# Optimization experiments

Hardware: AMD Instinct MI355X
Metric: run time of the kernel (lower is better)

Reference implementation:

```python
import jax, jax.numpy as jnp
import numpy as np

KERNEL_SIZE = 15


def setup_inputs() -> dict:
    key = jax.random.key(0)
    k1, k2 = jax.random.split(key)
    N, H, W = 16, 512, 512
    x = jax.random.normal(k1, (N, N, H, W), dtype=jnp.float32)
    kernel = jax.random.uniform(k2, (N, N, KERNEL_SIZE, KERNEL_SIZE), dtype=jnp.float32)
    return {"x": x, "kernel": kernel}


def reference(x, kernel):
    # x: (N, C, H, W) with b == c == N; kernel: (N, N, k, k)
    k = kernel.shape[-1]
    p = k // 2
    xs = x[:, 0:1, :, :]  # only channel 0 is used: (N, 1, H, W)
    xp = jnp.pad(xs, ((0, 0), (0, 0), (p, p), (p, p)), mode="reflect")  # ReflectionPad2d

    def per_sample(im, ker):
        # im: (1, Hp, Wp), ker: (N, k, k) -> conv of one image with N kernels
        o = jax.lax.conv_general_dilated(
            im[None],              # (1, 1, Hp, Wp)
            ker[:, None],          # (N, 1, k, k)
            window_strides=(1, 1),
            padding="VALID",
            dimension_numbers=("NCHW", "OIHW", "NCHW"),
        )[0]                       # (N, H, W)
        return o / jnp.max(o)      # global max-normalize per sample

    res = jax.vmap(per_sample)(xp, kernel)   # (i=N, j=N, H, W); res[i, j] = conv(x_i, kernel[i, j]) / max_j
    # original writes out[j, i] = res[i, j]
    return jnp.transpose(res, (1, 0, 2, 3))
```

## Files before the change

### kernel.cpp

```cpp
#include <hip/hip_runtime.h>

typedef __bf16 bf16x8 __attribute__((ext_vector_type(8)));
typedef float f32x4 __attribute__((ext_vector_type(4)));
typedef unsigned int u32;
typedef unsigned short u16;

#define PDIM 528
#define PIMG (PDIM * PDIM)
#define IN_STRIDE 56
#define IN_ROWS   31

__device__ __forceinline__ u16 f2bf(float f) {
    u32 u = __builtin_bit_cast(u32, f);
    return (u16)((u + 0x7FFFu + ((u >> 16) & 1u)) >> 16);
}
__device__ __forceinline__ int refl(int i) {
    return i < 0 ? -i : (i > 511 ? 1022 - i : i);
}

__global__ __launch_bounds__(256) void cvtpad(const float* __restrict__ x,
                                              u16* __restrict__ P) {
    const int u  = blockIdx.x * 256 + threadIdx.x;
    const int n  = u / (PDIM * 66);
    const int r  = u - n * (PDIM * 66);
    const int pr = r / 66;
    const int cs = r - pr * 66;
    const int pc0 = cs * 8;
    const float* sx = x + (size_t)n * (16u * 512u * 512u) + (size_t)refl(pr - 7) * 512;
    const int g0 = pc0 - 8;
    float v[8];
    if (g0 >= 0 && g0 <= 504) {
        const float4 a = *(const float4*)(sx + g0);
        const float4 b = *(const float4*)(sx + g0 + 4);
        v[0] = a.x; v[1] = a.y; v[2] = a.z; v[3] = a.w;
        v[4] = b.x; v[5] = b.y; v[6] = b.z; v[7] = b.w;
    } else {
        #pragma unroll
        for (int i = 0; i < 8; ++i) v[i] = sx[refl(g0 + i)];
    }
    uint4 q;
    q.x = (u32)f2bf(v[0]) | ((u32)f2bf(v[1]) << 16);
    q.y = (u32)f2bf(v[2]) | ((u32)f2bf(v[3]) << 16);
    q.z = (u32)f2bf(v[4]) | ((u32)f2bf(v[5]) << 16);
    q.w = (u32)f2bf(v[6]) | ((u32)f2bf(v[7]) << 16);
    *(uint4*)(P + (size_t)n * PIMG + (size_t)pr * PDIM + pc0) = q;
}

__global__ __launch_bounds__(256) void packkern(const float* __restrict__ kern,
                                                uint4* __restrict__ afragG) {
    const int u = blockIdx.x * 256 + threadIdx.x;
    const int n    = u >> 9;
    const int rem  = u & 511;
    const int ks   = rem >> 6;
    const int lane = rem & 63;
    const int oca = lane & 15, g = lane >> 4, g1 = g & 1, g2 = g >> 1;
    const float* kp = kern + ((size_t)n * 16 + oca) * 225;
    const int kh = 2 * ks + g2;
    u16 b[8];
    #pragma unroll
    for (int j = 0; j < 8; ++j) {
        const int kw = 8 * g1 + j;
        b[j] = f2bf((kh < 15 && kw < 15) ? kp[kh * 15 + kw] : 0.f);
    }
    uint4 q;
    q.x = (u32)b[0] | ((u32)b[1] << 16);
    q.y = (u32)b[2] | ((u32)b[3] << 16);
    q.z = (u32)b[4] | ((u32)b[5] << 16);
    q.w = (u32)b[6] | ((u32)b[7] << 16);
    afragG[u] = q;
}

template <int MODE>
__global__ __launch_bounds__(256) void dynconv(const u16* __restrict__ P,
                                               const uint4* __restrict__ afragG,
                                               float* __restrict__ out,
                                               float* __restrict__ partial) {
    __shared__ __align__(16) u16 lds_in[IN_ROWS * IN_STRIDE];
    __shared__ float wm[4];

    const int tid  = threadIdx.x;
    const int lane = tid & 63;
    const int wave = tid >> 6;
    const int c0 = blockIdx.x * 32;
    const int h0 = blockIdx.y * 16;
    const int n  = blockIdx.z;

    if (tid < IN_ROWS * 6) {
        const int rr  = tid / 6;
        const int cs8 = tid - rr * 6;
        const uint4 q = *(const uint4*)(P + (size_t)n * PIMG
                                        + (size_t)(h0 + rr) * PDIM + c0 + 8 * cs8);
        *(uint4*)&lds_in[rr * IN_STRIDE + 8 * cs8] = q;
    }

    const int g  = lane >> 4;
    const int g1 = g & 1;
    const int g2 = g >> 1;
    bf16x8 afrag[8];
    {
        const uint4* ap = afragG + ((size_t)n << 9) + lane;
        #pragma unroll
        for (int ks = 0; ks < 8; ++ks)
            afrag[ks] = __builtin_bit_cast(bf16x8, ap[ks << 6]);
    }

    float scale = 0.f;
    if constexpr (MODE == 1) {
        const float* pp = partial + n * 512 + lane * 8;
        const float4 a = *(const float4*)pp;
        const float4 b = *(const float4*)(pp + 4);
        float pv = fmaxf(fmaxf(fmaxf(a.x, a.y), fmaxf(a.z, a.w)),
                         fmaxf(fmaxf(b.x, b.y), fmaxf(b.z, b.w)));
        #pragma unroll
        for (int off = 32; off > 0; off >>= 1) pv = fmaxf(pv, __shfl_xor(pv, off, 64));
        scale = 1.0f / pv;
    }

    __syncthreads();

    const int hh = lane & 15;
    const char* lbase = (const char*)lds_in
                        + (hh + g2) * (IN_STRIDE * 2) + 16 * (wave + g1);

    f32x4 acc[8];
    #pragma unroll
    for (int t = 0; t < 8; ++t) acc[t] = f32x4{0.f, 0.f, 0.f, 0.f};

    u32 Ea[8], Eb[8];
#define LDE(E, ks) do {                                                        \
        const uint4 _a = *(const uint4*)(lbase + (ks) * (2 * IN_STRIDE * 2));  \
        const uint4 _b = *(const uint4*)(lbase + (ks) * (2 * IN_STRIDE * 2) + 16); \
        E[0] = _a.x; E[1] = _a.y; E[2] = _a.z; E[3] = _a.w;                    \
        E[4] = _b.x; E[5] = _b.y; E[6] = _b.z; E[7] = _b.w; } while (0)
#define KSTEP(E, ks) do {                                                      \
        _Pragma("unroll")                                                      \
        for (int t = 0; t < 8; ++t) {                                          \
            const int s = t + 1, xb = s >> 1;                                  \
            u32 d0, d1, d2, d3;                                                \
            if (s & 1) {                                                       \
                d0 = __builtin_amdgcn_alignbit(E[xb + 1], E[xb], 16);          \
                d1 = __builtin_amdgcn_alignbit(E[xb + 2], E[xb + 1], 16);      \
                d2 = __builtin_amdgcn_alignbit(E[xb + 3], E[xb + 2], 16);      \
                d3 = __builtin_amdgcn_alignbit(E[xb + 4], E[xb + 3], 16);      \
            } else { d0 = E[xb]; d1 = E[xb + 1]; d2 = E[xb + 2]; d3 = E[xb + 3]; } \
            uint4 dv; dv.x = d0; dv.y = d1; dv.z = d2; dv.w = d3;              \
            acc[t] = __builtin_amdgcn_mfma_f32_16x16x32_bf16(                  \
                afrag[ks], __builtin_bit_cast(bf16x8, dv), acc[t], 0, 0, 0);   \
        } } while (0)

    LDE(Ea, 0);
    LDE(Eb, 1); KSTEP(Ea, 0);
    LDE(Ea, 2); KSTEP(Eb, 1);
    LDE(Eb, 3); KSTEP(Ea, 2);
    LDE(Ea, 4); KSTEP(Eb, 3);
    LDE(Eb, 5); KSTEP(Ea, 4);
    LDE(Ea, 6); KSTEP(Eb, 5);
    LDE(Eb, 7); KSTEP(Ea, 6);
    KSTEP(Eb, 7);
#undef LDE
#undef KSTEP

    if constexpr (MODE == 0) {
        float m = -3.4e38f;
        #pragma unroll
        for (int t = 0; t < 8; ++t)
            #pragma unroll
            for (int r = 0; r < 4; ++r) m = fmaxf(m, acc[t][r]);
        #pragma unroll
        for (int off = 32; off > 0; off >>= 1) m = fmaxf(m, __shfl_xor(m, off, 64));
        if (lane == 0) wm[wave] = m;
        __syncthreads();
        if (tid == 0)
            partial[n * 512 + blockIdx.y * 16 + blockIdx.x] =
                fmaxf(fmaxf(wm[0], wm[1]), fmaxf(wm[2], wm[3]));
    } else {
        __shared__ __align__(16) float lout[4 * 16 * 36];
        const int oh_w  = g * 16 + hh;
        float* wp = &lout[oh_w * 36 + ((8 * wave) ^ (8 * (oh_w & 3)))];
        const int oh_r = tid >> 2;
        const int ci   = (tid & 3) * 8;
        const float* rp = &lout[oh_r * 36 + (ci ^ (8 * (oh_r & 3)))];
        const int oc2 = oh_r >> 4, h2 = oh_r & 15;

        #pragma unroll
        for (int r = 0; r < 4; ++r) {
            __syncthreads();
            f32x4 v0, v1;
            v0[0] = acc[0][r] * scale; v0[1] = acc[1][r] * scale;
            v0[2] = acc[2][r] * scale; v0[3] = acc[3][r] * scale;
            v1[0] = acc[4][r] * scale; v1[1] = acc[5][r] * scale;
            v1[2] = acc[6][r] * scale; v1[3] = acc[7][r] * scale;
            *(f32x4*)wp       = v0;
            *(f32x4*)(wp + 4) = v1;
            __syncthreads();
            const f32x4 s0 = *(const f32x4*)rp;
            const f32x4 s1 = *(const f32x4*)(rp + 4);
            float* orow = out + (((size_t)((4 * oc2 + r) * 16 + n)) * 512
                                 + (size_t)(h0 + h2)) * 512 + c0 + ci;
            *(f32x4*)orow       = s0;
            *(f32x4*)(orow + 4) = s1;
        }
    }
}

extern "C" void kernel_launch(void* const* d_in, const int* in_sizes, int n_in,
                              void* d_out, int out_size, void* d_ws, size_t ws_size,
                              hipStream_t stream) {
    (void)in_sizes; (void)n_in; (void)out_size; (void)ws_size;
    const float* x  = (const float*)d_in[0];
    const float* k  = (const float*)d_in[1];
    float* out      = (float*)d_out;
    u16* P          = (u16*)d_ws;
    uint4* afragG   = (uint4*)((char*)d_ws + (10u << 20));
    float* partial  = (float*)((char*)d_ws + (12u << 20));

    cvtpad<<<dim3(16 * PDIM * 66 / 256), dim3(256), 0, stream>>>(x, P);
    packkern<<<dim3(32), dim3(256), 0, stream>>>(k, afragG);
    dim3 grid(16, 32, 16);
    dim3 block(256);
    dynconv<0><<<grid, block, 0, stream>>>(P, afragG, out, partial);
    dynconv<1><<<grid, block, 0, stream>>>(P, afragG, out, partial);
}
```

Before: 108.3 us.

## Merge prepass kernels and store four pre-shifted input copies in LDS

Combines the input convert/pad kernel and the kernel-weight packing kernel into one launch, saving a kernel launch. In the conv kernel, the input tile is staged into LDS as four copies shifted by 0-3 bf16 elements, so each MFMA operand becomes a direct LDS load instead of a register alignbit shuffle. This removes per-step VALU shifting from the inner loop. In exchange it uses four times the LDS, issues more LDS reads (some split into two 8-byte loads), and does extra work during staging.

```diff
diff --git a/kernel.cpp b/kernel.cpp
--- a/kernel.cpp
+++ b/kernel.cpp
@@ -7,8 +7,9 @@
 
 #define PDIM 528
 #define PIMG (PDIM * PDIM)
-#define IN_STRIDE 56
-#define IN_ROWS   31
+#define ROW_B   112
+#define COPY_B  (31 * ROW_B)
+#define NCVT 2178
 
 __device__ __forceinline__ u16 f2bf(float f) {
     u32 u = __builtin_bit_cast(u32, f);
@@ -18,56 +19,58 @@
     return i < 0 ? -i : (i > 511 ? 1022 - i : i);
 }
 
-__global__ __launch_bounds__(256) void cvtpad(const float* __restrict__ x,
-                                              u16* __restrict__ P) {
-    const int u  = blockIdx.x * 256 + threadIdx.x;
-    const int n  = u / (PDIM * 66);
-    const int r  = u - n * (PDIM * 66);
-    const int pr = r / 66;
-    const int cs = r - pr * 66;
-    const int pc0 = cs * 8;
-    const float* sx = x + (size_t)n * (16u * 512u * 512u) + (size_t)refl(pr - 7) * 512;
-    const int g0 = pc0 - 8;
-    float v[8];
-    if (g0 >= 0 && g0 <= 504) {
-        const float4 a = *(const float4*)(sx + g0);
-        const float4 b = *(const float4*)(sx + g0 + 4);
-        v[0] = a.x; v[1] = a.y; v[2] = a.z; v[3] = a.w;
-        v[4] = b.x; v[5] = b.y; v[6] = b.z; v[7] = b.w;
+__global__ __launch_bounds__(256) void prepass(const float* __restrict__ x,
+                                               const float* __restrict__ kern,
+                                               u16* __restrict__ P,
+                                               uint4* __restrict__ afragG) {
+    if (blockIdx.x < NCVT) {
+        const int u  = blockIdx.x * 256 + threadIdx.x;
+        const int n  = u / (PDIM * 66);
+        const int r  = u - n * (PDIM * 66);
+        const int pr = r / 66;
+        const int cs = r - pr * 66;
+        const int pc0 = cs * 8;
+        const float* sx = x + (size_t)n * (16u * 512u * 512u)
+                          + (size_t)refl(pr - 7) * 512;
+        const int g0 = pc0 - 8;
+        float v[8];
+        if (g0 >= 0 && g0 <= 504) {
+            const float4 a = *(const float4*)(sx + g0);
+            const float4 b = *(const float4*)(sx + g0 + 4);
+            v[0] = a.x; v[1] = a.y; v[2] = a.z; v[3] = a.w;
+            v[4] = b.x; v[5] = b.y; v[6] = b.z; v[7] = b.w;
+        } else {
+            #pragma unroll
+            for (int i = 0; i < 8; ++i) v[i] = sx[refl(g0 + i)];
+        }
+        uint4 q;
+        q.x = (u32)f2bf(v[0]) | ((u32)f2bf(v[1]) << 16);
+        q.y = (u32)f2bf(v[2]) | ((u32)f2bf(v[3]) << 16);
+        q.z = (u32)f2bf(v[4]) | ((u32)f2bf(v[5]) << 16);
+        q.w = (u32)f2bf(v[6]) | ((u32)f2bf(v[7]) << 16);
+        *(uint4*)(P + (size_t)n * PIMG + (size_t)pr * PDIM + pc0) = q;
     } else {
-        #pragma unroll
-        for (int i = 0; i < 8; ++i) v[i] = sx[refl(g0 + i)];
-    }
-    uint4 q;
-    q.x = (u32)f2bf(v[0]) | ((u32)f2bf(v[1]) << 16);
-    q.y = (u32)f2bf(v[2]) | ((u32)f2bf(v[3]) << 16);
-    q.z = (u32)f2bf(v[4]) | ((u32)f2bf(v[5]) << 16);
-    q.w = (u32)f2bf(v[6]) | ((u32)f2bf(v[7]) << 16);
-    *(uint4*)(P + (size_t)n * PIMG + (size_t)pr * PDIM + pc0) = q;
-}
-
-__global__ __launch_bounds__(256) void packkern(const float* __restrict__ kern,
-                                                uint4* __restrict__ afragG) {
-    const int u = blockIdx.x * 256 + threadIdx.x;
-    const int n    = u >> 9;
-    const int rem  = u & 511;
-    const int ks   = rem >> 6;
-    const int lane = rem & 63;
-    const int oca = lane & 15, g = lane >> 4, g1 = g & 1, g2 = g >> 1;
-    const float* kp = kern + ((size_t)n * 16 + oca) * 225;
-    const int kh = 2 * ks + g2;
-    u16 b[8];
-    #pragma unroll
-    for (int j = 0; j < 8; ++j) {
-        const int kw = 8 * g1 + j;
-        b[j] = f2bf((kh < 15 && kw < 15) ? kp[kh * 15 + kw] : 0.f);
-    }
-    uint4 q;
-    q.x = (u32)b[0] | ((u32)b[1] << 16);
-    q.y = (u32)b[2] | ((u32)b[3] << 16);
-    q.z = (u32)b[4] | ((u32)b[5] << 16);
-    q.w = (u32)b[6] | ((u32)b[7] << 16);
-    afragG[u] = q;
+        const int u = (blockIdx.x - NCVT) * 256 + threadIdx.x;
+        const int n    = u >> 9;
+        const int rem  = u & 511;
+        const int ks   = rem >> 6;
+        const int lane = rem & 63;
+        const int oca = lane & 15, g = lane >> 4, g1 = g & 1, g2 = g >> 1;
+        const float* kp = kern + ((size_t)n * 16 + oca) * 225;
+        const int kh = 2 * ks + g2;
+        u16 b[8];
+        #pragma unroll
+        for (int j = 0; j < 8; ++j) {
+            const int kw = 8 * g1 + j;
+            b[j] = f2bf((kh < 15 && kw < 15) ? kp[kh * 15 + kw] : 0.f);
+        }
+        uint4 q;
+        q.x = (u32)b[0] | ((u32)b[1] << 16);
+        q.y = (u32)b[2] | ((u32)b[3] << 16);
+        q.z = (u32)b[4] | ((u32)b[5] << 16);
+        q.w = (u32)b[6] | ((u32)b[7] << 16);
+        afragG[u] = q;
+    }
 }
 
 template <int MODE>
@@ -75,7 +78,7 @@
                                                const uint4* __restrict__ afragG,
                                                float* __restrict__ out,
                                                float* __restrict__ partial) {
-    __shared__ __align__(16) u16 lds_in[IN_ROWS * IN_STRIDE];
+    __shared__ __align__(16) char lds4[4 * COPY_B];
     __shared__ float wm[4];
 
     const int tid  = threadIdx.x;
@@ -85,12 +88,29 @@
     const int h0 = blockIdx.y * 16;
     const int n  = blockIdx.z;
 
-    if (tid < IN_ROWS * 6) {
-        const int rr  = tid / 6;
-        const int cs8 = tid - rr * 6;
-        const uint4 q = *(const uint4*)(P + (size_t)n * PIMG
-                                        + (size_t)(h0 + rr) * PDIM + c0 + 8 * cs8);
-        *(uint4*)&lds_in[rr * IN_STRIDE + 8 * cs8] = q;
+    if (tid < 31 * 6) {
+        const int rr = tid / 6;
+        const int cs = tid - rr * 6;
+        const u16* src = P + (size_t)n * PIMG + (size_t)(h0 + rr) * PDIM + c0 + 8 * cs;
+        const uint4 A = *(const uint4*)(src);
+        const uint4 B = *(const uint4*)(src + 8);
+        const u32 W[6] = {A.x, A.y, A.z, A.w, B.x, B.y};
+        char* dst = lds4 + rr * ROW_B + 16 * cs;
+        uint4 q0, q1, q2, q3;
+        q0.x = W[0]; q0.y = W[1]; q0.z = W[2]; q0.w = W[3];
+        q1.x = __builtin_amdgcn_alignbit(W[1], W[0], 16);
+        q1.y = __builtin_amdgcn_alignbit(W[2], W[1], 16);
+        q1.z = __builtin_amdgcn_alignbit(W[3], W[2], 16);
+        q1.w = __builtin_amdgcn_alignbit(W[4], W[3], 16);
+        q2.x = W[1]; q2.y = W[2]; q2.z = W[3]; q2.w = W[4];
+        q3.x = __builtin_amdgcn_alignbit(W[2], W[1], 16);
+        q3.y = __builtin_amdgcn_alignbit(W[3], W[2], 16);
+        q3.z = __builtin_amdgcn_alignbit(W[4], W[3], 16);
+        q3.w = __builtin_amdgcn_alignbit(W[5], W[4], 16);
+        *(uint4*)(dst)              = q0;
+        *(uint4*)(dst + COPY_B)     = q1;
+        *(uint4*)(dst + 2 * COPY_B) = q2;
+        *(uint4*)(dst + 3 * COPY_B) = q3;
     }
 
     const int g  = lane >> 4;
@@ -119,46 +139,32 @@
     __syncthreads();
 
     const int hh = lane & 15;
-    const char* lbase = (const char*)lds_in
-                        + (hh + g2) * (IN_STRIDE * 2) + 16 * (wave + g1);
+    const char* lb = lds4 + (hh + g2) * ROW_B + 16 * (wave + g1);
 
     f32x4 acc[8];
     #pragma unroll
     for (int t = 0; t < 8; ++t) acc[t] = f32x4{0.f, 0.f, 0.f, 0.f};
 
-    u32 Ea[8], Eb[8];
-#define LDE(E, ks) do {                                                        \
-        const uint4 _a = *(const uint4*)(lbase + (ks) * (2 * IN_STRIDE * 2));  \
-        const uint4 _b = *(const uint4*)(lbase + (ks) * (2 * IN_STRIDE * 2) + 16); \
-        E[0] = _a.x; E[1] = _a.y; E[2] = _a.z; E[3] = _a.w;                    \
-        E[4] = _b.x; E[5] = _b.y; E[6] = _b.z; E[7] = _b.w; } while (0)
-#define KSTEP(E, ks) do {                                                      \
-        _Pragma("unroll")                                                      \
-        for (int t = 0; t < 8; ++t) {                                          \
-            const int s = t + 1, xb = s >> 1;                                  \
-            u32 d0, d1, d2, d3;                                                \
-            if (s & 1) {                                                       \
-                d0 = __builtin_amdgcn_alignbit(E[xb + 1], E[xb], 16);          \
-                d1 = __builtin_amdgcn_alignbit(E[xb + 2], E[xb + 1], 16);      \
-                d2 = __builtin_amdgcn_alignbit(E[xb + 3], E[xb + 2], 16);      \
-                d3 = __builtin_amdgcn_alignbit(E[xb + 4], E[xb + 3], 16);      \
-            } else { d0 = E[xb]; d1 = E[xb + 1]; d2 = E[xb + 2]; d3 = E[xb + 3]; } \
-            uint4 dv; dv.x = d0; dv.y = d1; dv.z = d2; dv.w = d3;              \
-            acc[t] = __builtin_amdgcn_mfma_f32_16x16x32_bf16(                  \
-                afrag[ks], __builtin_bit_cast(bf16x8, dv), acc[t], 0, 0, 0);   \
-        } } while (0)
-
-    LDE(Ea, 0);
-    LDE(Eb, 1); KSTEP(Ea, 0);
-    LDE(Ea, 2); KSTEP(Eb, 1);
-    LDE(Eb, 3); KSTEP(Ea, 2);
-    LDE(Ea, 4); KSTEP(Eb, 3);
-    LDE(Eb, 5); KSTEP(Ea, 4);
-    LDE(Ea, 6); KSTEP(Eb, 5);
-    LDE(Eb, 7); KSTEP(Ea, 6);
-    KSTEP(Eb, 7);
-#undef LDE
-#undef KSTEP
+    #pragma unroll
+    for (int ks = 0; ks < 8; ++ks) {
+        #pragma unroll
+        for (int t = 0; t < 8; ++t) {
+            const int s  = t + 1;
+            const int c  = s & 3;
+            const int sh = s - c;
+            const int off = c * COPY_B + ks * (2 * ROW_B) + 2 * sh;
+            uint4 dv;
+            if ((sh & 4) == 0) {
+                dv = *(const uint4*)(lb + off);
+            } else {
+                const uint2 lo = *(const uint2*)(lb + off);
+                const uint2 hi = *(const uint2*)(lb + off + 8);
+                dv.x = lo.x; dv.y = lo.y; dv.z = hi.x; dv.w = hi.y;
+            }
+            acc[t] = __builtin_amdgcn_mfma_f32_16x16x32_bf16(
+                afrag[ks], __builtin_bit_cast(bf16x8, dv), acc[t], 0, 0, 0);
+        }
+    }
 
     if constexpr (MODE == 0) {
         float m = -3.4e38f;
@@ -214,8 +220,7 @@
     uint4* afragG   = (uint4*)((char*)d_ws + (10u << 20));
     float* partial  = (float*)((char*)d_ws + (12u << 20));
 
-    cvtpad<<<dim3(16 * PDIM * 66 / 256), dim3(256), 0, stream>>>(x, P);
-    packkern<<<dim3(32), dim3(256), 0, stream>>>(k, afragG);
+    prepass<<<dim3(NCVT + 32), dim3(256), 0, stream>>>(x, k, P, afragG);
     dim3 grid(16, 32, 16);
     dim3 block(256);
     dynconv<0><<<grid, block, 0, stream>>>(P, afragG, out, partial);
```

Result: slower. 113.6 us (+4.9%).
